# Kernel optimization log

Measured on AMD Instinct MI355X. Metric: run time of the kernel, lower is better.

## Reference

```python
import jax, jax.numpy as jnp
import numpy as np

B, T, R = 128, 20, 49           # batch, caption length, num regions (7x7)
V, E, H, FD, A = 10000, 512, 512, 512, 256  # vocab, embed, hidden, feature, attn dims


def setup_inputs() -> dict:
    key = jax.random.key(0)
    ks = jax.random.split(key, 16)
    s = 0.02
    return {
        "features": jax.random.normal(ks[0], (B, R, FD), dtype=jnp.float32),
        "captions": jax.random.randint(ks[1], (B, T), 0, V),
        "emb": jax.random.normal(ks[2], (V, E), dtype=jnp.float32) * s,
        "W_h": jax.random.normal(ks[3], (A, H), dtype=jnp.float32) * s,
        "b_h": jnp.zeros((A,), jnp.float32),
        "W_f": jax.random.normal(ks[4], (A, FD), dtype=jnp.float32) * s,
        "b_f": jnp.zeros((A,), jnp.float32),
        "v_w": jax.random.normal(ks[5], (A,), dtype=jnp.float32) * s,
        "v_b": jnp.zeros((), jnp.float32),
        "W_ih": jax.random.normal(ks[6], (4 * H, E + FD), dtype=jnp.float32) * s,
        "W_hh": jax.random.normal(ks[7], (4 * H, H), dtype=jnp.float32) * s,
        "b_ih": jnp.zeros((4 * H,), jnp.float32),
        "b_hh": jnp.zeros((4 * H,), jnp.float32),
        "fc_W": jax.random.normal(ks[8], (V, H), dtype=jnp.float32) * s,
        "fc_b": jnp.zeros((V,), jnp.float32),
    }


def reference(features, captions, emb, W_h, b_h, W_f, b_f, v_w, v_b,
              W_ih, W_hh, b_ih, b_hh, fc_W, fc_b):
    Bn = features.shape[0]
    Hd = W_hh.shape[1]
    # features are constant across timesteps -> project once (same math as per-step W_f(features))
    f_proj = jnp.einsum('brf,af->bra', features, W_f) + b_f  # (B,R,A)
    embeds = emb[captions[:, :-1]]                            # (B,T-1,E)
    xs = jnp.swapaxes(embeds, 0, 1)                           # (T-1,B,E)
    bias = b_ih + b_hh

    def step(carry, x_t):
        hx, cx = carry
        # Bahdanau attention
        h = hx @ W_h.T + b_h                                  # (B,A)
        scores = jnp.tanh(h[:, None, :] + f_proj) @ v_w + v_b  # (B,R)
        alpha = jax.nn.softmax(scores, axis=1)
        context = jnp.einsum('br,brf->bf', alpha, features)   # (B,FD)
        # LSTMCell (PyTorch gate order: i,f,g,o)
        lstm_in = jnp.concatenate([x_t, context], axis=1)     # (B,E+FD)
        gates = lstm_in @ W_ih.T + hx @ W_hh.T + bias         # (B,4H)
        i, f, g, o = jnp.split(gates, 4, axis=1)
        cx = jax.nn.sigmoid(f) * cx + jax.nn.sigmoid(i) * jnp.tanh(g)
        hx = jax.nn.sigmoid(o) * jnp.tanh(cx)
        logit = hx @ fc_W.T + fc_b                            # (B,V)
        return (hx, cx), logit

    init = (jnp.zeros((Bn, Hd), features.dtype), jnp.zeros((Bn, Hd), features.dtype))
    _, logits = jax.lax.scan(step, init, xs)                  # (T-1,B,V)
    return jnp.swapaxes(logits, 0, 1)                         # (B,T-1,V)
```

## Files before the change

### kernel.cpp

```cpp
#include <hip/hip_runtime.h>
#include <hip/hip_bf16.h>
#include <math.h>

#define NB 128
#define NT 20
#define NS 19
#define NR 49
#define NV 10000
#define NE 512
#define NH 512
#define NFD 512
#define NA 256
#define NG 2048
#define NK2 1024

typedef __bf16 bf16_t;
typedef bf16_t bf16x8 __attribute__((ext_vector_type(8)));
typedef bf16_t bf16x4 __attribute__((ext_vector_type(4)));
typedef float f32x4 __attribute__((ext_vector_type(4)));

__device__ __forceinline__ float sigm(float x) { return 1.f / (1.f + expf(-x)); }

__device__ __forceinline__ void cvt8(bf16_t* d, const float* s) {
    float4 a = *(const float4*)s;
    float4 b = *(const float4*)(s + 4);
    bf16x8 v;
    v[0] = (bf16_t)a.x; v[1] = (bf16_t)a.y; v[2] = (bf16_t)a.z; v[3] = (bf16_t)a.w;
    v[4] = (bf16_t)b.x; v[5] = (bf16_t)b.y; v[6] = (bf16_t)b.z; v[7] = (bf16_t)b.w;
    *(bf16x8*)d = v;
}

__global__ __launch_bounds__(256) void k_prep(
    const float* __restrict__ fc_W, const float* __restrict__ W_ih,
    const float* __restrict__ W_hh, const float* __restrict__ W_h,
    const float* __restrict__ W_f, const float* __restrict__ features,
    const float* __restrict__ emb, const int* __restrict__ captions,
    const float* __restrict__ b_ih, const float* __restrict__ b_hh,
    const float* __restrict__ b_f, const float* __restrict__ b_h,
    bf16_t* __restrict__ fcWb, bf16_t* __restrict__ Wcat2,
    bf16_t* __restrict__ Wxg, bf16_t* __restrict__ W_hb,
    bf16_t* __restrict__ Wfb, bf16_t* __restrict__ featb,
    bf16_t* __restrict__ linx, float* __restrict__ bias,
    float* __restrict__ bfh, float* __restrict__ hx, float* __restrict__ cx,
    unsigned* __restrict__ flags)
{
    int g = blockIdx.x * 256 + threadIdx.x;
    if (g < 640000) { int idx = g * 8; cvt8(fcWb + idx, fc_W + idx); return; }
    g -= 640000;
    if (g < 262144) {
        int idx = g * 8;
        int row = idx >> 10, col = idx & 1023;
        int orig = (row & 3) * NH + (row >> 2);
        const float* src = (col < 512) ? (W_ih + (size_t)orig * 1024 + 512 + col)
                                       : (W_hh + (size_t)orig * 512 + (col - 512));
        cvt8(Wcat2 + idx, src);
        return;
    }
    g -= 262144;
    if (g < 131072) {
        int idx = g * 8;
        int row = idx >> 9, col = idx & 511;
        int orig = (row & 3) * NH + (row >> 2);
        cvt8(Wxg + idx, W_ih + (size_t)orig * 1024 + col);
        return;
    }
    g -= 131072;
    if (g < 16384) { int idx = g * 8; cvt8(W_hb + idx, W_h + idx); return; }
    g -= 16384;
    if (g < 16384) { int idx = g * 8; cvt8(Wfb + idx, W_f + idx); return; }
    g -= 16384;
    if (g < 401408) { int idx = g * 8; cvt8(featb + idx, features + idx); return; }
    g -= 401408;
    if (g < 155648) {
        int idx = g * 8;
        int row = idx >> 9, col = idx & 511;
        int t = row >> 7, b = row & 127;
        int cap = captions[b * NT + t];
        cvt8(linx + idx, emb + (size_t)cap * NE + col);
        return;
    }
    g -= 155648;
    if (g < 256) {
        int n0 = g * 8;
        #pragma unroll
        for (int i = 0; i < 8; ++i) {
            int n = n0 + i, h = n >> 2, gg = n & 3;
            int orig = gg * NH + h;
            bias[n] = b_ih[orig] + b_hh[orig];
        }
        return;
    }
    g -= 256;
    if (g < 32) {
        int n0 = g * 8;
        #pragma unroll
        for (int i = 0; i < 8; ++i) bfh[n0 + i] = b_f[n0 + i] + b_h[n0 + i];
        return;
    }
    g -= 32;
    float4 z = make_float4(0.f, 0.f, 0.f, 0.f);
    if (g < 8192) { *(float4*)(hx + g * 8) = z; *(float4*)(hx + g * 8 + 4) = z; return; }
    g -= 8192;
    if (g < 8192) { *(float4*)(cx + g * 8) = z; *(float4*)(cx + g * 8 + 4) = z; return; }
    g -= 8192;
    if (g < 304) {
        #pragma unroll
        for (int i = 0; i < 8; ++i) flags[g * 8 + i] = 0u;
    }
}

__global__ __launch_bounds__(256) void gemm_bf16_nt(
    const bf16_t* __restrict__ Am, const bf16_t* __restrict__ Bm,
    const float* __restrict__ bias, float* __restrict__ Cf,
    bf16_t* __restrict__ Cb, int M, int N, int K, int ldc)
{
    __shared__ uint4 AsU[512];
    __shared__ uint4 BsU[512];
    int tid = threadIdx.x;
    int m0 = blockIdx.x * 64, n0 = blockIdx.y * 64;
    int nk = K >> 6;

    int rowS = tid >> 3, slotS = tid & 7;
    int wr0 = rowS * 8 + (slotS ^ (rowS & 7));
    int rowS2 = rowS + 32;
    int wr1 = rowS2 * 8 + (slotS ^ (rowS2 & 7));

    const uint4* pA = (const uint4*)(Am + (size_t)(m0 + rowS) * K) + slotS;
    size_t aStep = (size_t)4 * K;
    int nrow0 = n0 + rowS, nrow1 = n0 + rowS2;
    bool bv0 = nrow0 < N, bv1 = nrow1 < N;
    const uint4* pB0 = (const uint4*)(Bm + (size_t)nrow0 * K) + slotS;
    const uint4* pB1 = (const uint4*)(Bm + (size_t)nrow1 * K) + slotS;
    uint4 zz = make_uint4(0, 0, 0, 0);

    int w = tid >> 6, lane = tid & 63;
    int wm = w >> 1, wn = w & 1;
    int lr = lane & 15, lg = lane >> 4;
    int ra[2][2], rb[2][2];
    #pragma unroll
    for (int i = 0; i < 2; ++i)
        #pragma unroll
        for (int kk = 0; kk < 2; ++kk) {
            int rA = wm * 32 + i * 16 + lr;
            int rB = wn * 32 + i * 16 + lr;
            int s = kk * 4 + lg;
            ra[i][kk] = rA * 8 + (s ^ (rA & 7));
            rb[i][kk] = rB * 8 + (s ^ (rB & 7));
        }

    f32x4 acc00 = {}, acc01 = {}, acc10 = {}, acc11 = {};
    uint4 a0 = pA[0], a1 = pA[aStep];
    uint4 b0 = bv0 ? pB0[0] : zz;
    uint4 b1 = bv1 ? pB1[0] : zz;
    pA += 8; pB0 += 8; pB1 += 8;

    #pragma unroll 1
    for (int kt = 0; kt < nk; ++kt) {
        __syncthreads();
        AsU[wr0] = a0; AsU[wr1] = a1;
        BsU[wr0] = b0; BsU[wr1] = b1;
        if (kt + 1 < nk) {
            a0 = pA[0]; a1 = pA[aStep];
            b0 = bv0 ? pB0[0] : zz;
            b1 = bv1 ? pB1[0] : zz;
            pA += 8; pB0 += 8; pB1 += 8;
        }
        __syncthreads();
        const bf16x8* Af = (const bf16x8*)AsU;
        const bf16x8* Bf = (const bf16x8*)BsU;
        #pragma unroll
        for (int kk = 0; kk < 2; ++kk) {
            bf16x8 fa0 = Af[ra[0][kk]], fa1 = Af[ra[1][kk]];
            bf16x8 fb0 = Bf[rb[0][kk]], fb1 = Bf[rb[1][kk]];
            acc00 = __builtin_amdgcn_mfma_f32_16x16x32_bf16(fa0, fb0, acc00, 0, 0, 0);
            acc01 = __builtin_amdgcn_mfma_f32_16x16x32_bf16(fa0, fb1, acc01, 0, 0, 0);
            acc10 = __builtin_amdgcn_mfma_f32_16x16x32_bf16(fa1, fb0, acc10, 0, 0, 0);
            acc11 = __builtin_amdgcn_mfma_f32_16x16x32_bf16(fa1, fb1, acc11, 0, 0, 0);
        }
    }

    f32x4 av[2][2] = {{acc00, acc01}, {acc10, acc11}};
    #pragma unroll
    for (int i = 0; i < 2; ++i) {
        int mbase = m0 + wm * 32 + i * 16 + lg * 4;
        #pragma unroll
        for (int j = 0; j < 2; ++j) {
            int n = n0 + wn * 32 + j * 16 + lr;
            if (n < N) {
                float bz = bias ? bias[n] : 0.f;
                #pragma unroll
                for (int r = 0; r < 4; ++r) {
                    float v = av[i][j][r] + bz;
                    if (Cb) Cb[(size_t)(mbase + r) * ldc + n] = (bf16_t)v;
                    else    Cf[(size_t)(mbase + r) * ldc + n] = v;
                }
            }
        }
    }
}

__global__ __launch_bounds__(512) void k_attn(
    const float* __restrict__ hx, const bf16_t* __restrict__ W_hb,
    const bf16_t* __restrict__ fprojb, const float* __restrict__ v_w,
    const bf16_t* __restrict__ featb, bf16_t* __restrict__ lin)
{
    int b = blockIdx.x;
    int tid = threadIdx.x;
    int w = tid >> 6, lane = tid & 63;
    __shared__ float hxs[NH];
    __shared__ float part[2][NA];
    __shared__ float salpha[64];

    hxs[tid] = hx[b * NH + tid];
    __syncthreads();

    {
        int a = tid & 255, q = tid >> 8;
        const bf16x8* wrow = (const bf16x8*)(W_hb + (size_t)a * NH + q * 256);
        const float* hq = hxs + q * 256;
        float p = 0.f;
        #pragma unroll
        for (int c = 0; c < 32; ++c) {
            bf16x8 wv = wrow[c];
            int k = c * 8;
            p += hq[k+0]*(float)wv[0] + hq[k+1]*(float)wv[1]
               + hq[k+2]*(float)wv[2] + hq[k+3]*(float)wv[3]
               + hq[k+4]*(float)wv[4] + hq[k+5]*(float)wv[5]
               + hq[k+6]*(float)wv[6] + hq[k+7]*(float)wv[7];
        }
        part[q][a] = p;
    }
    __syncthreads();

    {
        for (int r = w; r < NR; r += 8) {
            const bf16_t* fp = fprojb + ((size_t)b * NR + r) * NA;
            float s = 0.f;
            #pragma unroll
            for (int j = 0; j < 4; ++j) {
                int aa = lane + 64 * j;
                float hv = part[0][aa] + part[1][aa];
                s += tanhf(hv + (float)fp[aa]) * v_w[aa];
            }
            #pragma unroll
            for (int off = 32; off; off >>= 1) s += __shfl_xor(s, off);
            if (lane == 0) salpha[r] = s;
        }
    }
    __syncthreads();

    if (tid < 64) {
        float v = (tid < NR) ? salpha[tid] : -INFINITY;
        float m = v;
        #pragma unroll
        for (int off = 32; off; off >>= 1) m = fmaxf(m, __shfl_xor(m, off));
        float e = (tid < NR) ? expf(v - m) : 0.f;
        float ssum = e;
        #pragma unroll
        for (int off = 32; off; off >>= 1) ssum += __shfl_xor(ssum, off);
        if (tid < NR) salpha[tid] = e / ssum;
    }
    __syncthreads();

    {
        bf16_t* lrow = lin + (size_t)b * NK2;
        float c = 0.f;
        #pragma unroll 7
        for (int r = 0; r < NR; ++r)
            c += salpha[r] * (float)featb[((size_t)b * NR + r) * NFD + tid];
        lrow[tid] = (bf16_t)c;
        lrow[NFD + tid] = (bf16_t)hxs[tid];
    }
}

__global__ __launch_bounds__(512) void k_fused(
    bf16_t* lin,
    const bf16_t* __restrict__ Wcat2, const bf16_t* __restrict__ pre_x,
    const float* __restrict__ bias, float* hx,
    float* __restrict__ cx, bf16_t* __restrict__ hxAll,
    const bf16_t* __restrict__ W_hb, const bf16_t* __restrict__ fprojb,
    const float* __restrict__ v_w, const bf16_t* __restrict__ featb,
    unsigned* flags, int t, int last)
{
    __shared__ __align__(16) char smem[20736];
    uint4* AsU = (uint4*)smem;
    uint4* BsU = AsU + 256;

    int tid = threadIdx.x;
    int xcd = blockIdx.x & 7, loc = blockIdx.x >> 3;
    int jg = xcd * 4 + (loc & 3);
    int ig = loc >> 2;
    int m0 = ig * 32, n0 = jg * 64;

    int rowS = tid >> 3, slotS = tid & 7;
    int wrB = rowS * 8 + (slotS ^ (rowS & 7));
    bool hasA = rowS < 32;
    int arow = hasA ? (m0 + rowS) : m0;

    const uint4* pB = (const uint4*)(Wcat2 + (size_t)(n0 + rowS) * NK2) + slotS;
    const uint4* pA = (const uint4*)(lin + (size_t)arow * NK2) + slotS;

    int w = tid >> 6, lane = tid & 63;
    int wm = w & 1, wn = w >> 1;
    int lr = lane & 15, lg = lane >> 4;
    int raI[2], rbI[2];
    #pragma unroll
    for (int kk = 0; kk < 2; ++kk) {
        int s = kk * 4 + lg;
        int rA = wm * 16 + lr;
        int rB = wn * 16 + lr;
        raI[kk] = rA * 8 + (s ^ (rA & 7));
        rbI[kk] = rB * 8 + (s ^ (rB & 7));
    }

    f32x4 acc = {};
    uint4 aR = {}, bR = pB[0];
    if (hasA) aR = pA[0];
    pB += 8; pA += 8;

    #pragma unroll 1
    for (int kt = 0; kt < NK2 / 64; ++kt) {
        __syncthreads();
        BsU[wrB] = bR;
        if (hasA) AsU[wrB] = aR;
        if (kt + 1 < NK2 / 64) {
            bR = pB[0]; pB += 8;
            if (hasA) { aR = pA[0]; pA += 8; }
        }
        __syncthreads();
        const bf16x8* Af = (const bf16x8*)AsU;
        const bf16x8* Bf = (const bf16x8*)BsU;
        #pragma unroll
        for (int kk = 0; kk < 2; ++kk) {
            bf16x8 fa = Af[raI[kk]];
            bf16x8 fb = Bf[rbI[kk]];
            acc = __builtin_amdgcn_mfma_f32_16x16x32_bf16(fa, fb, acc, 0, 0, 0);
        }
    }

    __syncthreads();
    float* Ct = (float*)smem;
    {
        int crow = wm * 16 + lg * 4;
        int ccol = wn * 16 + lr;
        #pragma unroll
        for (int r = 0; r < 4; ++r)
            Ct[(crow + r) * 65 + ccol] = acc[r];
    }
    __syncthreads();

    {
        int hloc = tid & 15, m = tid >> 4;
        int bb2 = m0 + m;
        int h = (n0 >> 2) + hloc;
        const float* crow = Ct + m * 65 + hloc * 4;
        const float* brow = bias + n0 + hloc * 4;
        const bf16_t* prow = pre_x + ((size_t)t * NB + bb2) * NG + n0 + hloc * 4;
        float gi = crow[0] + brow[0] + (float)prow[0];
        float gf = crow[1] + brow[1] + (float)prow[1];
        float gg = crow[2] + brow[2] + (float)prow[2];
        float go = crow[3] + brow[3] + (float)prow[3];
        size_t idx = (size_t)bb2 * NH + h;
        float c = sigm(gf) * cx[idx] + sigm(gi) * tanhf(gg);
        float hn = sigm(go) * tanhf(c);
        cx[idx] = c;
        __hip_atomic_store(hx + idx, hn, __ATOMIC_RELAXED,
                           __HIP_MEMORY_SCOPE_AGENT);
        hxAll[((size_t)t * NB + bb2) * NH + h] = (bf16_t)hn;
    }
    if (last) return;

    __syncthreads();
    {
        unsigned* fl = flags + t * 128 + ig * 32;
        if (tid == 0)
            __hip_atomic_store(fl + jg, 1u, __ATOMIC_RELAXED,
                               __HIP_MEMORY_SCOPE_AGENT);
        if (tid < 32) {
            while (__hip_atomic_load(fl + tid, __ATOMIC_RELAXED,
                                     __HIP_MEMORY_SCOPE_AGENT) == 0u)
                __builtin_amdgcn_s_sleep(2);
        }
    }
    __syncthreads();

    int bb = m0 + jg;
    float* hxs  = (float*)smem;
    float* part = hxs + 512;
    float* salp = part + 512;
    float* ctxp = salp + 64;

    hxs[tid] = __hip_atomic_load(hx + (size_t)bb * NH + tid,
                                 __ATOMIC_RELAXED, __HIP_MEMORY_SCOPE_AGENT);
    __syncthreads();

    {
        int a = tid & 255, q = tid >> 8;
        const bf16x8* wrow = (const bf16x8*)(W_hb + (size_t)a * NH + q * 256);
        const float* hq = hxs + q * 256;
        float p = 0.f;
        #pragma unroll
        for (int c = 0; c < 32; ++c) {
            bf16x8 wv = wrow[c];
            int k = c * 8;
            p += hq[k+0]*(float)wv[0] + hq[k+1]*(float)wv[1]
               + hq[k+2]*(float)wv[2] + hq[k+3]*(float)wv[3]
               + hq[k+4]*(float)wv[4] + hq[k+5]*(float)wv[5]
               + hq[k+6]*(float)wv[6] + hq[k+7]*(float)wv[7];
        }
        part[q * 256 + a] = p;
    }
    __syncthreads();
    if (tid < 256) part[tid] += part[256 + tid];
    __syncthreads();

    {
        for (int r = w; r < NR; r += 8) {
            bf16x4 fp4 = *(const bf16x4*)(fprojb + ((size_t)bb * NR + r) * NA + lane * 4);
            float4 vw4 = *(const float4*)(v_w + lane * 4);
            const float* hb = part + lane * 4;
            float s = tanhf(hb[0] + (float)fp4[0]) * vw4.x
                    + tanhf(hb[1] + (float)fp4[1]) * vw4.y
                    + tanhf(hb[2] + (float)fp4[2]) * vw4.z
                    + tanhf(hb[3] + (float)fp4[3]) * vw4.w;
            #pragma unroll
            for (int off = 32; off; off >>= 1) s += __shfl_xor(s, off);
            if (lane == 0) salp[r] = s;
        }
    }
    __syncthreads();

    if (tid < 64) {
        float v = (tid < NR) ? salp[tid] : -INFINITY;
        float m = v;
        #pragma unroll
        for (int off = 32; off; off >>= 1) m = fmaxf(m, __shfl_xor(m, off));
        float e = (tid < NR) ? expf(v - m) : 0.f;
        float ssum = e;
        #pragma unroll
        for (int off = 32; off; off >>= 1) ssum += __shfl_xor(ssum, off);
        if (tid < NR) salp[tid] = e / ssum;
    }
    __syncthreads();

    {
        int ck = tid & 63, rg = tid >> 6;
        float c[8] = {};
        for (int r = rg; r < NR; r += 8) {
            bf16x8 v = *(const bf16x8*)(featb + ((size_t)bb * NR + r) * NFD + ck * 8);
            float al = salp[r];
            #pragma unroll
            for (int jj = 0; jj < 8; ++jj) c[jj] += al * (float)v[jj];
        }
        float* cp = ctxp + (rg * 64 + ck) * 8;
        #pragma unroll
        for (int jj = 0; jj < 8; ++jj) cp[jj] = c[jj];
    }
    __syncthreads();

    {
        float cc = 0.f;
        #pragma unroll
        for (int rg = 0; rg < 8; ++rg) cc += ctxp[rg * 512 + tid];
        bf16_t* lrow = lin + (size_t)bb * NK2;
        lrow[tid]       = (bf16_t)cc;
        lrow[512 + tid] = (bf16_t)hxs[tid];
    }
}

__global__ __launch_bounds__(256) void k_logits(
    const bf16_t* __restrict__ hxAll, const bf16_t* __restrict__ fcWb,
    const float* __restrict__ fc_b, float* __restrict__ out)
{
    const int NWG = 38 * 157, Q = NWG / 8, RR = NWG % 8;
    int bid = blockIdx.x;
    int xcd = bid & 7, loc = bid >> 3;
    int swz = (xcd < RR ? xcd * (Q + 1) : RR * (Q + 1) + (xcd - RR) * Q) + loc;
    int m0 = (swz % 38) * 64;
    int n0 = (swz / 38) * 64;

    __shared__ uint4 AsU[512];
    __shared__ uint4 BsU[512];
    int tid = threadIdx.x;

    int rowS = tid >> 3, slotS = tid & 7;
    int wr0 = rowS * 8 + (slotS ^ (rowS & 7));
    int rowS2 = rowS + 32;
    int wr1 = rowS2 * 8 + (slotS ^ (rowS2 & 7));

    const uint4* pA = (const uint4*)(hxAll + (size_t)(m0 + rowS) * NH) + slotS;
    size_t aStep = (size_t)4 * NH;
    int nrow0 = n0 + rowS, nrow1 = n0 + rowS2;
    bool bv0 = nrow0 < NV, bv1 = nrow1 < NV;
    const uint4* pB0 = (const uint4*)(fcWb + (size_t)nrow0 * NH) + slotS;
    const uint4* pB1 = (const uint4*)(fcWb + (size_t)nrow1 * NH) + slotS;
    uint4 zz = make_uint4(0, 0, 0, 0);

    int w = tid >> 6, lane = tid & 63;
    int wm = w >> 1, wn = w & 1;
    int lr = lane & 15, lg = lane >> 4;
    int ra[2][2], rb[2][2];
    #pragma unroll
    for (int i = 0; i < 2; ++i)
        #pragma unroll
        for (int kk = 0; kk < 2; ++kk) {
            int rA = wm * 32 + i * 16 + lr;
            int rB = wn * 32 + i * 16 + lr;
            int s = kk * 4 + lg;
            ra[i][kk] = rA * 8 + (s ^ (rA & 7));
            rb[i][kk] = rB * 8 + (s ^ (rB & 7));
        }

    f32x4 acc00 = {}, acc01 = {}, acc10 = {}, acc11 = {};
    uint4 a0 = pA[0], a1 = pA[aStep];
    uint4 b0 = bv0 ? pB0[0] : zz;
    uint4 b1 = bv1 ? pB1[0] : zz;
    pA += 8; pB0 += 8; pB1 += 8;

    #pragma unroll 1
    for (int kt = 0; kt < NH / 64; ++kt) {
        __syncthreads();
        AsU[wr0] = a0; AsU[wr1] = a1;
        BsU[wr0] = b0; BsU[wr1] = b1;
        if (kt + 1 < NH / 64) {
            a0 = pA[0]; a1 = pA[aStep];
            b0 = bv0 ? pB0[0] : zz;
            b1 = bv1 ? pB1[0] : zz;
            pA += 8; pB0 += 8; pB1 += 8;
        }
        __syncthreads();
        const bf16x8* Af = (const bf16x8*)AsU;
        const bf16x8* Bf = (const bf16x8*)BsU;
        #pragma unroll
        for (int kk = 0; kk < 2; ++kk) {
            bf16x8 fa0 = Af[ra[0][kk]], fa1 = Af[ra[1][kk]];
            bf16x8 fb0 = Bf[rb[0][kk]], fb1 = Bf[rb[1][kk]];
            acc00 = __builtin_amdgcn_mfma_f32_16x16x32_bf16(fa0, fb0, acc00, 0, 0, 0);
            acc01 = __builtin_amdgcn_mfma_f32_16x16x32_bf16(fa0, fb1, acc01, 0, 0, 0);
            acc10 = __builtin_amdgcn_mfma_f32_16x16x32_bf16(fa1, fb0, acc10, 0, 0, 0);
            acc11 = __builtin_amdgcn_mfma_f32_16x16x32_bf16(fa1, fb1, acc11, 0, 0, 0);
        }
    }

    f32x4 av[2][2] = {{acc00, acc01}, {acc10, acc11}};
    float* Ct = (float*)AsU;
    const int LDC = 68;
    int col4 = (tid & 15) * 4;
    int n = n0 + col4;
    bool nok = n < NV;
    f32x4 bz = {};
    if (nok) bz = *(const f32x4*)(fc_b + n);

    #pragma unroll
    for (int h = 0; h < 2; ++h) {
        __syncthreads();
        if (wm == h) {
            #pragma unroll
            for (int i = 0; i < 2; ++i) {
                int rloc = i * 16 + lg * 4;
                #pragma unroll
                for (int j = 0; j < 2; ++j) {
                    int cloc = wn * 32 + j * 16 + lr;
                    #pragma unroll
                    for (int r = 0; r < 4; ++r)
                        Ct[(rloc + r) * LDC + cloc] = av[i][j][r];
                }
            }
        }
        __syncthreads();
        if (nok) {
            #pragma unroll
            for (int p = 0; p < 2; ++p) {
                int rloc = p * 16 + (tid >> 4);
                int m = m0 + h * 32 + rloc;
                int bb = m & 127, tt = m >> 7;
                f32x4 v = *(const f32x4*)(Ct + rloc * LDC + col4);
                v += bz;
                __builtin_nontemporal_store(
                    v, (f32x4*)(out + ((size_t)bb * NS + tt) * NV + n));
            }
        }
    }
}

extern "C" void kernel_launch(void* const* d_in, const int* in_sizes, int n_in,
                              void* d_out, int out_size, void* d_ws, size_t ws_size,
                              hipStream_t stream)
{
    const float* features = (const float*)d_in[0];
    const int*   captions = (const int*)d_in[1];
    const float* emb      = (const float*)d_in[2];
    const float* W_h      = (const float*)d_in[3];
    const float* b_h      = (const float*)d_in[4];
    const float* W_f      = (const float*)d_in[5];
    const float* b_f      = (const float*)d_in[6];
    const float* v_w      = (const float*)d_in[7];
    const float* W_ih     = (const float*)d_in[9];
    const float* W_hh     = (const float*)d_in[10];
    const float* b_ih     = (const float*)d_in[11];
    const float* b_hh     = (const float*)d_in[12];
    const float* fc_W     = (const float*)d_in[13];
    const float* fc_b     = (const float*)d_in[14];
    float* out = (float*)d_out;

    char* base = (char*)d_ws;
    bf16_t* fcWb   = (bf16_t*)base;  base += (size_t)NV * NH * 2;
    bf16_t* Wcat2  = (bf16_t*)base;  base += (size_t)NG * NK2 * 2;
    bf16_t* Wxg    = (bf16_t*)base;  base += (size_t)NG * NE * 2;
    bf16_t* W_hb   = (bf16_t*)base;  base += (size_t)NA * NH * 2;
    bf16_t* Wfb    = (bf16_t*)base;  base += (size_t)NA * NFD * 2;
    bf16_t* featb  = (bf16_t*)base;  base += (size_t)NB * NR * NFD * 2;
    bf16_t* linx   = (bf16_t*)base;  base += (size_t)NS * NB * NE * 2;
    bf16_t* pre_x  = (bf16_t*)base;  base += (size_t)NS * NB * NG * 2;
    bf16_t* lin    = (bf16_t*)base;  base += (size_t)NB * NK2 * 2;
    bf16_t* hxAll  = (bf16_t*)base;  base += (size_t)NS * NB * NH * 2;
    bf16_t* fprojb = (bf16_t*)base;  base += (size_t)NB * NR * NA * 2;
    float*  bias   = (float*)base;   base += (size_t)NG * 4;
    float*  bfh    = (float*)base;   base += (size_t)NA * 4;
    float*  hx     = (float*)base;   base += (size_t)NB * NH * 4;
    float*  cx     = (float*)base;   base += (size_t)NB * NH * 4;
    unsigned* flags = (unsigned*)base; base += (size_t)NS * 128 * 4;

    k_prep<<<dim3(6407), 256, 0, stream>>>(
        fc_W, W_ih, W_hh, W_h, W_f, features, emb, captions, b_ih, b_hh,
        b_f, b_h, fcWb, Wcat2, Wxg, W_hb, Wfb, featb, linx, bias, bfh,
        hx, cx, flags);

    gemm_bf16_nt<<<dim3(98, 4), 256, 0, stream>>>(
        featb, Wfb, bfh, (float*)0, fprojb, NB * NR, NA, NFD, NA);

    gemm_bf16_nt<<<dim3(38, 32), 256, 0, stream>>>(
        linx, Wxg, (const float*)0, (float*)0, pre_x, NS * NB, NG, NE, NG);

    k_attn<<<dim3(NB), 512, 0, stream>>>(hx, W_hb, fprojb, v_w, featb, lin);

    for (int t = 0; t < NS; ++t) {
        k_fused<<<dim3(128), 512, 0, stream>>>(
            lin, Wcat2, pre_x, bias, hx, cx, hxAll,
            W_hb, fprojb, v_w, featb, flags, t, (t == NS - 1) ? 1 : 0);
    }

    k_logits<<<dim3(38 * 157), 256, 0, stream>>>(hxAll, fcWb, fc_b, out);
}
```

Before: 548.8 us.

## Split recurrent step into 256 smaller workgroups with half doing attention

The per-timestep fused LSTM+attention kernel now launches 256 workgroups of 256 threads, each computing a 16x64 gate tile instead of 32x64. Half of the workgroups then run the attention for one batch row each, while the rest exit after signalling their flag. The flag array and its initialisation are doubled to match the new row grouping. The aim is to spread the serial recurrence over more compute units and shorten each block's critical path, at the cost of more synchronisation flags and idle blocks during attention.

```diff
diff --git a/kernel.cpp b/kernel.cpp
--- a/kernel.cpp
+++ b/kernel.cpp
@@ -103,7 +103,7 @@
     g -= 8192;
     if (g < 8192) { *(float4*)(cx + g * 8) = z; *(float4*)(cx + g * 8 + 4) = z; return; }
     g -= 8192;
-    if (g < 304) {
+    if (g < 608) {
         #pragma unroll
         for (int i = 0; i < 8; ++i) flags[g * 8 + i] = 0u;
     }
@@ -273,7 +273,7 @@
     }
 }
 
-__global__ __launch_bounds__(512) void k_fused(
+__global__ __launch_bounds__(256) void k_step2(
     bf16_t* lin,
     const bf16_t* __restrict__ Wcat2, const bf16_t* __restrict__ pre_x,
     const float* __restrict__ bias, float* hx,
@@ -282,50 +282,52 @@
     const float* __restrict__ v_w, const bf16_t* __restrict__ featb,
     unsigned* flags, int t, int last)
 {
-    __shared__ __align__(16) char smem[20736];
+    __shared__ __align__(16) char smem[11584];
     uint4* AsU = (uint4*)smem;
-    uint4* BsU = AsU + 256;
+    uint4* BsU = AsU + 128;
 
     int tid = threadIdx.x;
     int xcd = blockIdx.x & 7, loc = blockIdx.x >> 3;
     int jg = xcd * 4 + (loc & 3);
     int ig = loc >> 2;
-    int m0 = ig * 32, n0 = jg * 64;
-
-    int rowS = tid >> 3, slotS = tid & 7;
-    int wrB = rowS * 8 + (slotS ^ (rowS & 7));
-    bool hasA = rowS < 32;
-    int arow = hasA ? (m0 + rowS) : m0;
-
-    const uint4* pB = (const uint4*)(Wcat2 + (size_t)(n0 + rowS) * NK2) + slotS;
-    const uint4* pA = (const uint4*)(lin + (size_t)arow * NK2) + slotS;
+    int m0 = ig * 16, n0 = jg * 64;
+
+    int rB0 = tid >> 3, sl = tid & 7;
+    int rB1 = rB0 + 32;
+    int wrB0 = rB0 * 8 + (sl ^ (rB0 & 7));
+    int wrB1 = rB1 * 8 + (sl ^ (rB1 & 7));
+    bool hasA = tid < 128;
+    int rA_ = tid >> 3;
+    int wrA = rA_ * 8 + (sl ^ (rA_ & 7));
+
+    const uint4* pB0 = (const uint4*)(Wcat2 + (size_t)(n0 + rB0) * NK2) + sl;
+    const uint4* pB1 = (const uint4*)(Wcat2 + (size_t)(n0 + rB1) * NK2) + sl;
+    const uint4* pA  = (const uint4*)(lin + (size_t)(m0 + (hasA ? rA_ : 0)) * NK2) + sl;
 
     int w = tid >> 6, lane = tid & 63;
-    int wm = w & 1, wn = w >> 1;
     int lr = lane & 15, lg = lane >> 4;
     int raI[2], rbI[2];
     #pragma unroll
     for (int kk = 0; kk < 2; ++kk) {
         int s = kk * 4 + lg;
-        int rA = wm * 16 + lr;
-        int rB = wn * 16 + lr;
-        raI[kk] = rA * 8 + (s ^ (rA & 7));
+        int rB = w * 16 + lr;
+        raI[kk] = lr * 8 + (s ^ (lr & 7));
         rbI[kk] = rB * 8 + (s ^ (rB & 7));
     }
 
     f32x4 acc = {};
-    uint4 aR = {}, bR = pB[0];
-    if (hasA) aR = pA[0];
-    pB += 8; pA += 8;
+    uint4 b0 = pB0[0], b1 = pB1[0], a0 = {};
+    if (hasA) a0 = pA[0];
+    pB0 += 8; pB1 += 8; pA += 8;
 
     #pragma unroll 1
     for (int kt = 0; kt < NK2 / 64; ++kt) {
         __syncthreads();
-        BsU[wrB] = bR;
-        if (hasA) AsU[wrB] = aR;
+        BsU[wrB0] = b0; BsU[wrB1] = b1;
+        if (hasA) AsU[wrA] = a0;
         if (kt + 1 < NK2 / 64) {
-            bR = pB[0]; pB += 8;
-            if (hasA) { aR = pA[0]; pA += 8; }
+            b0 = pB0[0]; b1 = pB1[0]; pB0 += 8; pB1 += 8;
+            if (hasA) { a0 = pA[0]; pA += 8; }
         }
         __syncthreads();
         const bf16x8* Af = (const bf16x8*)AsU;
@@ -341,8 +343,8 @@
     __syncthreads();
     float* Ct = (float*)smem;
     {
-        int crow = wm * 16 + lg * 4;
-        int ccol = wn * 16 + lr;
+        int crow = lg * 4;
+        int ccol = w * 16 + lr;
         #pragma unroll
         for (int r = 0; r < 4; ++r)
             Ct[(crow + r) * 65 + ccol] = acc[r];
@@ -371,54 +373,54 @@
     if (last) return;
 
     __syncthreads();
-    {
-        unsigned* fl = flags + t * 128 + ig * 32;
-        if (tid == 0)
-            __hip_atomic_store(fl + jg, 1u, __ATOMIC_RELAXED,
-                               __HIP_MEMORY_SCOPE_AGENT);
-        if (tid < 32) {
-            while (__hip_atomic_load(fl + tid, __ATOMIC_RELAXED,
-                                     __HIP_MEMORY_SCOPE_AGENT) == 0u)
-                __builtin_amdgcn_s_sleep(2);
-        }
-    }
-    __syncthreads();
-
-    int bb = m0 + jg;
+    unsigned* fl = flags + t * 256 + ig * 32;
+    if (tid == 0)
+        __hip_atomic_store(fl + jg, 1u, __ATOMIC_RELAXED,
+                           __HIP_MEMORY_SCOPE_AGENT);
+
+    bool doA = (loc & 3) < 2;
+    if (!doA) return;
+
+    if (tid < 32) {
+        while (__hip_atomic_load(fl + tid, __ATOMIC_RELAXED,
+                                 __HIP_MEMORY_SCOPE_AGENT) == 0u)
+            __builtin_amdgcn_s_sleep(2);
+    }
+    __syncthreads();
+
+    int bb = m0 + xcd * 2 + (loc & 3);
     float* hxs  = (float*)smem;
-    float* part = hxs + 512;
-    float* salp = part + 512;
+    float* hatt = hxs + 512;
+    float* salp = hatt + 256;
     float* ctxp = salp + 64;
 
-    hxs[tid] = __hip_atomic_load(hx + (size_t)bb * NH + tid,
+    hxs[tid]       = __hip_atomic_load(hx + (size_t)bb * NH + tid,
                                  __ATOMIC_RELAXED, __HIP_MEMORY_SCOPE_AGENT);
-    __syncthreads();
-
-    {
-        int a = tid & 255, q = tid >> 8;
-        const bf16x8* wrow = (const bf16x8*)(W_hb + (size_t)a * NH + q * 256);
-        const float* hq = hxs + q * 256;
+    hxs[tid + 256] = __hip_atomic_load(hx + (size_t)bb * NH + tid + 256,
+                                 __ATOMIC_RELAXED, __HIP_MEMORY_SCOPE_AGENT);
+    __syncthreads();
+
+    {
+        const bf16x8* wrow = (const bf16x8*)(W_hb + (size_t)tid * NH);
         float p = 0.f;
         #pragma unroll
-        for (int c = 0; c < 32; ++c) {
+        for (int c = 0; c < 64; ++c) {
             bf16x8 wv = wrow[c];
             int k = c * 8;
-            p += hq[k+0]*(float)wv[0] + hq[k+1]*(float)wv[1]
-               + hq[k+2]*(float)wv[2] + hq[k+3]*(float)wv[3]
-               + hq[k+4]*(float)wv[4] + hq[k+5]*(float)wv[5]
-               + hq[k+6]*(float)wv[6] + hq[k+7]*(float)wv[7];
-        }
-        part[q * 256 + a] = p;
-    }
-    __syncthreads();
-    if (tid < 256) part[tid] += part[256 + tid];
-    __syncthreads();
-
-    {
-        for (int r = w; r < NR; r += 8) {
+            p += hxs[k+0]*(float)wv[0] + hxs[k+1]*(float)wv[1]
+               + hxs[k+2]*(float)wv[2] + hxs[k+3]*(float)wv[3]
+               + hxs[k+4]*(float)wv[4] + hxs[k+5]*(float)wv[5]
+               + hxs[k+6]*(float)wv[6] + hxs[k+7]*(float)wv[7];
+        }
+        hatt[tid] = p;
+    }
+    __syncthreads();
+
+    {
+        for (int r = w; r < NR; r += 4) {
             bf16x4 fp4 = *(const bf16x4*)(fprojb + ((size_t)bb * NR + r) * NA + lane * 4);
             float4 vw4 = *(const float4*)(v_w + lane * 4);
-            const float* hb = part + lane * 4;
+            const float* hb = hatt + lane * 4;
             float s = tanhf(hb[0] + (float)fp4[0]) * vw4.x
                     + tanhf(hb[1] + (float)fp4[1]) * vw4.y
                     + tanhf(hb[2] + (float)fp4[2]) * vw4.z
@@ -446,7 +448,7 @@
     {
         int ck = tid & 63, rg = tid >> 6;
         float c[8] = {};
-        for (int r = rg; r < NR; r += 8) {
+        for (int r = rg; r < NR; r += 4) {
             bf16x8 v = *(const bf16x8*)(featb + ((size_t)bb * NR + r) * NFD + ck * 8);
             float al = salp[r];
             #pragma unroll
@@ -459,12 +461,15 @@
     __syncthreads();
 
     {
-        float cc = 0.f;
-        #pragma unroll
-        for (int rg = 0; rg < 8; ++rg) cc += ctxp[rg * 512 + tid];
         bf16_t* lrow = lin + (size_t)bb * NK2;
-        lrow[tid]       = (bf16_t)cc;
-        lrow[512 + tid] = (bf16_t)hxs[tid];
+        #pragma unroll
+        for (int p2 = 0; p2 < 2; ++p2) {
+            int col = tid + p2 * 256;
+            float cc = ctxp[col] + ctxp[512 + col]
+                     + ctxp[1024 + col] + ctxp[1536 + col];
+            lrow[col]       = (bf16_t)cc;
+            lrow[512 + col] = (bf16_t)hxs[col];
+        }
     }
 }
 
@@ -619,9 +624,9 @@
     float*  bfh    = (float*)base;   base += (size_t)NA * 4;
     float*  hx     = (float*)base;   base += (size_t)NB * NH * 4;
     float*  cx     = (float*)base;   base += (size_t)NB * NH * 4;
-    unsigned* flags = (unsigned*)base; base += (size_t)NS * 128 * 4;
-
-    k_prep<<<dim3(6407), 256, 0, stream>>>(
+    unsigned* flags = (unsigned*)base; base += (size_t)NS * 256 * 4;
+
+    k_prep<<<dim3(6408), 256, 0, stream>>>(
         fc_W, W_ih, W_hh, W_h, W_f, features, emb, captions, b_ih, b_hh,
         b_f, b_h, fcWb, Wcat2, Wxg, W_hb, Wfb, featb, linx, bias, bfh,
         hx, cx, flags);
@@ -635,7 +640,7 @@
     k_attn<<<dim3(NB), 512, 0, stream>>>(hx, W_hb, fprojb, v_w, featb, lin);
 
     for (int t = 0; t < NS; ++t) {
-        k_fused<<<dim3(128), 512, 0, stream>>>(
+        k_step2<<<dim3(256), 256, 0, stream>>>(
             lin, Wcat2, pre_x, bias, hx, cx, hxAll,
             W_hb, fprojb, v_w, featb, flags, t, (t == NS - 1) ? 1 : 0);
     }
```

New measurement: 646.4 us. 1.18x slower.
